# Performance work log

Hardware: AMD Instinct MI355X
Metric: run time of the kernel (lower is better)

The kernel has to match this reference:

```python
import jax, jax.numpy as jnp
import numpy as np

B = 16384
D = 1024          # fusion_hidden == depth_hidden == expert hidden
ORD_H = 512       # max(48, fusion_hidden // 2)
E = 7             # num_size_classes (= number of depth experts)
C_SIZE = 7        # num_size_classes
C_DEPTH = 3       # num_depth_classes


def _lin(key, fan_in, fan_out):
    return jax.random.normal(key, (fan_in, fan_out), dtype=jnp.float32) / np.sqrt(fan_in)


def setup_inputs() -> dict:
    key = jax.random.key(0)
    ks = jax.random.split(key, 16)
    inp = {
        'hybrid_feat': jax.random.normal(ks[0], (B, D), dtype=jnp.float32),
        # size_cls_head: Linear(D, D) -> ReLU -> Linear(D, 7)
        'Wc1': _lin(ks[1], D, D), 'bc1': jnp.zeros((D,), jnp.float32),
        'Wc2': _lin(ks[2], D, C_SIZE), 'bc2': jnp.zeros((C_SIZE,), jnp.float32),
        # size_ord_head: Linear(D, 512) -> ReLU -> Linear(512, 6)
        'Wo1': _lin(ks[3], D, ORD_H), 'bo1': jnp.zeros((ORD_H,), jnp.float32),
        'Wo2': _lin(ks[4], ORD_H, C_SIZE - 1), 'bo2': jnp.zeros((C_SIZE - 1,), jnp.float32),
        # size_residual_head: Linear(D, D) -> ReLU -> Linear(D, 1)
        'Wr1': _lin(ks[5], D, D), 'br1': jnp.zeros((D,), jnp.float32),
        'Wr2': _lin(ks[6], D, 1), 'br2': jnp.zeros((1,), jnp.float32),
        # depth_adapter: Linear(D, D) -> ReLU
        'Wa': _lin(ks[7], D, D), 'ba': jnp.zeros((D,), jnp.float32),
        # 7 stacked DepthExperts: Linear(D,D) ReLU Linear(D,D) ReLU Linear(D,3)
        'We1': jax.random.normal(ks[8], (E, D, D), jnp.float32) / np.sqrt(D),
        'be1': jnp.zeros((E, D), jnp.float32),
        'We2': jax.random.normal(ks[9], (E, D, D), jnp.float32) / np.sqrt(D),
        'be2': jnp.zeros((E, D), jnp.float32),
        'We3': jax.random.normal(ks[10], (E, D, C_DEPTH), jnp.float32) / np.sqrt(D),
        'be3': jnp.zeros((E, C_DEPTH), jnp.float32),
    }
    return inp


def reference(hybrid_feat, Wc1, bc1, Wc2, bc2, Wo1, bo1, Wo2, bo2,
              Wr1, br1, Wr2, br2, Wa, ba, We1, be1, We2, be2, We3, be3):
    x = hybrid_feat  # [B, D]
    relu = jax.nn.relu
    # size classification head
    size_logits = relu(x @ Wc1 + bc1) @ Wc2 + bc2                      # [B, 7]
    # ordinal head
    size_ord_logits = relu(x @ Wo1 + bo1) @ Wo2 + bo2                  # [B, 6]
    size_probs = jax.nn.softmax(size_logits, axis=1)                   # [B, 7]
    size_values = jnp.linspace(0.0, 1.0, C_SIZE, dtype=size_probs.dtype)
    expected_norm = jnp.sum(size_probs * size_values[None, :], axis=1, keepdims=True)  # [B, 1]
    residual = 0.35 * jnp.tanh(relu(x @ Wr1 + br1) @ Wr2 + br2)        # [B, 1]
    size_reg_norm = jnp.clip(expected_norm + residual, 0.0, 1.0)       # [B, 1]
    # depth adapter + hard-routed depth experts (route_depth_logits)
    depth_feat = relu(x @ Wa + ba)                                     # [B, D]
    size_idx = jnp.argmax(size_logits, axis=1)                         # [B] hard route
    # dense all-expert compute, then per-row select == gather/scatter dispatch
    h1 = relu(jnp.einsum('bd,edh->ebh', depth_feat, We1) + be1[:, None, :])   # [E, B, D]
    h2 = relu(jnp.einsum('ebd,edh->ebh', h1, We2) + be2[:, None, :])          # [E, B, D]
    expert_logits = jnp.einsum('ebd,edc->ebc', h2, We3) + be3[:, None, :]     # [E, B, 3]
    depth_logits = jnp.take_along_axis(
        jnp.transpose(expert_logits, (1, 0, 2)),  # [B, E, 3]
        size_idx[:, None, None], axis=1)[:, 0, :]                       # [B, 3]
    # single concatenated output: [B, 7 + 6 + 1 + 7 + 3] = [B, 24]
    return jnp.concatenate(
        [size_logits, size_ord_logits, size_reg_norm, size_probs, depth_logits], axis=1)
```

## Files before the change

### kernel.cpp

```cpp
#include <hip/hip_runtime.h>
#include <cstdint>
#include <cstddef>

typedef unsigned short u16;
typedef u16 u16x8 __attribute__((ext_vector_type(8)));
typedef __bf16 bf16x8 __attribute__((ext_vector_type(8)));
typedef float f32x4 __attribute__((ext_vector_type(4)));

#define B_ROWS 16384
#define DIM 1024
#define ORDH 512
#define NEXP 7
#define NFUSE 2560

__device__ __forceinline__ u16 f2bf(float f) {
  unsigned u = __builtin_bit_cast(unsigned, f);
  u += 0x7FFFu + ((u >> 16) & 1u);
  return (u16)(u >> 16);
}
__device__ __forceinline__ float bf2f(u16 h) {
  return __builtin_bit_cast(float, ((unsigned)h) << 16);
}

typedef __attribute__((address_space(1))) const void gas_void;
typedef __attribute__((address_space(3))) void las_void;
__device__ __forceinline__ void gload16(const void* g, void* l) {
  __builtin_amdgcn_global_load_lds((gas_void*)g, (las_void*)l, 16, 0, 0);
}

__global__ __launch_bounds__(256) void convert_x_kernel(
    const float4* __restrict__ x, ushort4* __restrict__ xh,
    ushort4* __restrict__ xl, int* __restrict__ gcnt, int* __restrict__ cursor) {
  if (blockIdx.x == 0 && threadIdx.x < 2 * NEXP) {
    if (threadIdx.x < NEXP) gcnt[threadIdx.x] = 0;
    else cursor[threadIdx.x - NEXP] = 0;
  }
  const int i = blockIdx.x * 256 + threadIdx.x;
  float4 v = x[i];
  ushort4 h, l;
  h.x = f2bf(v.x); l.x = f2bf(v.x - bf2f(h.x));
  h.y = f2bf(v.y); l.y = f2bf(v.y - bf2f(h.y));
  h.z = f2bf(v.z); l.z = f2bf(v.z - bf2f(h.z));
  h.w = f2bf(v.w); l.w = f2bf(v.w - bf2f(h.w));
  xh[i] = h; xl[i] = l;
}

__global__ __launch_bounds__(256) void transpose_all_kernel(
    const float* __restrict__ Wc1, u16* __restrict__ Tc1h, u16* __restrict__ Tc1l,
    const float* __restrict__ Wo1, u16* __restrict__ To1,
    const float* __restrict__ Wr1, u16* __restrict__ Tr1,
    const float* __restrict__ Wa,  u16* __restrict__ Ta,
    const float* __restrict__ We1, u16* __restrict__ Te1,
    const float* __restrict__ We2, u16* __restrict__ Te2) {
  __shared__ float tile[32][33];
  int bid = blockIdx.x;
  const float* W; u16* H; u16* L = nullptr;
  int N = 1024, bx, by;
  size_t zoff = 0;
  if (bid < 1024)      { W = Wc1; H = Tc1h; L = Tc1l; bx = bid & 31; by = bid >> 5; }
  else if (bid < 1536) { bid -= 1024; W = Wo1; H = To1; N = 512; bx = bid & 15; by = bid >> 4; }
  else if (bid < 2560) { bid -= 1536; W = Wr1; H = Tr1; bx = bid & 31; by = bid >> 5; }
  else if (bid < 3584) { bid -= 2560; W = Wa; H = Ta; bx = bid & 31; by = bid >> 5; }
  else if (bid < 10752){ bid -= 3584; W = We1; H = Te1;
                         zoff = (size_t)(bid >> 10) * DIM * DIM; bid &= 1023;
                         bx = bid & 31; by = bid >> 5; }
  else                 { bid -= 10752; W = We2; H = Te2;
                         zoff = (size_t)(bid >> 10) * DIM * DIM; bid &= 1023;
                         bx = bid & 31; by = bid >> 5; }
  const int K = 1024;
  const int bk = by * 32, bn = bx * 32;
  const int tx = threadIdx.x & 31, ty = threadIdx.x >> 5;
#pragma unroll
  for (int r = 0; r < 32; r += 8)
    tile[ty + r][tx] = W[zoff + (size_t)(bk + ty + r) * N + (bn + tx)];
  __syncthreads();
#pragma unroll
  for (int r = 0; r < 32; r += 8) {
    const float v = tile[tx][ty + r];
    const size_t o = zoff + (size_t)(bn + ty + r) * K + (bk + tx);
    const u16 h = f2bf(v);
    H[o] = h;
    if (L) L[o] = f2bf(v - bf2f(h));
  }
}

__device__ __forceinline__ void gemm_loop(
    const u16* __restrict__ aP0, const u16* __restrict__ bP0,
    const u16* __restrict__ aP1, const u16* __restrict__ bP1,
    const u16* __restrict__ aP2, const u16* __restrict__ bP2,
    int npass, int K, int m0, int n0, u16* SM, int tid, f32x4 (&acc)[4][4]) {
  const int lane = tid & 63;
  const int w = tid >> 6;
  const int wm = w >> 1, wn = w & 1;
  const int sRow = tid >> 3, sSlot = tid & 7;
  const int ldsOff = sRow * 64 + sSlot * 8;
  const size_t aOff = (size_t)(m0 + sRow) * K + ((sSlot ^ (sRow & 7)) * 8);
  const size_t bOff = (size_t)(n0 + sRow) * K + ((sSlot ^ (sRow & 7)) * 8);
  const u16* aCur = aP0 + aOff;
  const u16* bCur = bP0 + bOff;
  int sp = 0, sk = 0;
  auto stageNext = [&](int b) {
    u16* d = SM + b * 16384 + ldsOff;
    const u16* as = aCur + sk;
    const u16* bs = bCur + sk;
#pragma unroll
    for (int r = 0; r < 4; ++r) {
      gload16(as + (size_t)(r * 32) * K, d + r * 32 * 64);
      gload16(bs + (size_t)(r * 32) * K, d + 8192 + r * 32 * 64);
    }
    sk += 64;
    if (sk == K) {
      sk = 0; ++sp;
      if (sp == 1) { aCur = aP1 + aOff; bCur = bP1 + bOff; }
      else         { aCur = aP2 + aOff; bCur = bP2 + bOff; }
    }
  };

  const int ntiles = npass * (K >> 6);
  stageNext(0);
  int cur = 0;
  for (int ti = 0; ti < ntiles; ++ti) {
    if (ti + 1 < ntiles) {
      stageNext(cur ^ 1);
      asm volatile("s_waitcnt vmcnt(8)\n\ts_barrier" ::: "memory");
    } else {
      asm volatile("s_waitcnt vmcnt(0)\n\ts_barrier" ::: "memory");
    }
    const u16* As = SM + cur * 16384;
    const u16* Bs = As + 8192;
#pragma unroll
    for (int s = 0; s < 2; ++s) {
      const int cAx = s * 4 + (lane >> 4);
      const int colO = (cAx ^ (lane & 7)) * 8;
      bf16x8 af[4], bfr[4];
#pragma unroll
      for (int t = 0; t < 4; ++t) {
        const int rowA = wm * 64 + t * 16 + (lane & 15);
        af[t] = __builtin_bit_cast(bf16x8, *(const u16x8*)&As[rowA * 64 + colO]);
        const int rowB = wn * 64 + t * 16 + (lane & 15);
        bfr[t] = __builtin_bit_cast(bf16x8, *(const u16x8*)&Bs[rowB * 64 + colO]);
      }
      __builtin_amdgcn_s_setprio(1);
#pragma unroll
      for (int mt = 0; mt < 4; ++mt)
#pragma unroll
        for (int nt = 0; nt < 4; ++nt)
          acc[mt][nt] = __builtin_amdgcn_mfma_f32_16x16x32_bf16(
              af[mt], bfr[nt], acc[mt][nt], 0, 0, 0);
      __builtin_amdgcn_s_setprio(0);
    }
    asm volatile("s_barrier" ::: "memory");
    cur ^= 1;
  }
}

__global__ __launch_bounds__(256, 2) void mgemm_bt_kernel(
    const u16* __restrict__ A0, const u16* __restrict__ B0,
    const u16* __restrict__ A1, const u16* __restrict__ B1,
    const u16* __restrict__ A2, const u16* __restrict__ B2,
    int npass, int K,
    float* __restrict__ outF, const float* __restrict__ biasF, int ldoF,
    u16* __restrict__ o0, u16* __restrict__ o1, u16* __restrict__ o2,
    const float* __restrict__ b0, const float* __restrict__ b1,
    const float* __restrict__ b2) {
  __shared__ __attribute__((aligned(16))) u16 SM[4 * 128 * 64];
  const int tid = threadIdx.x;
  const int lane = tid & 63;
  const int w = tid >> 6;
  const int wm = w >> 1, wn = w & 1;
  const unsigned nwg = gridDim.x * gridDim.y;
  const unsigned wgid = blockIdx.y * gridDim.x + blockIdx.x;
  const unsigned swz = (wgid & 7u) * (nwg >> 3) + (wgid >> 3);
  const int m0 = (int)(swz / gridDim.x) * 128;
  const int n0 = (int)(swz % gridDim.x) * 128;

  f32x4 acc[4][4] = {};
  gemm_loop(A0, B0, A1, B1, A2, B2, npass, K, m0, n0, SM, tid, acc);

  const int q = lane >> 4, cl = lane & 15;
#pragma unroll
  for (int nt = 0; nt < 4; ++nt) {
    const int col = n0 + wn * 64 + nt * 16 + cl;
    if (outF) {
      const float bv = biasF[col];
#pragma unroll
      for (int mt = 0; mt < 4; ++mt)
#pragma unroll
        for (int i = 0; i < 4; ++i) {
          const int row = m0 + wm * 64 + mt * 16 + q * 4 + i;
          float v = acc[mt][nt][i] + bv;
          outF[(size_t)row * ldoF + col] = v > 0.f ? v : 0.f;
        }
    } else {
      u16* ob; const float* bp; int lc, ld;
      if (col < ORDH)            { ob = o0; bp = b0; lc = col;               ld = ORDH; }
      else if (col < ORDH + DIM) { ob = o1; bp = b1; lc = col - ORDH;        ld = DIM; }
      else                       { ob = o2; bp = b2; lc = col - (ORDH + DIM); ld = DIM; }
      const float bv = bp[lc];
#pragma unroll
      for (int mt = 0; mt < 4; ++mt)
#pragma unroll
        for (int i = 0; i < 4; ++i) {
          const int row = m0 + wm * 64 + mt * 16 + q * 4 + i;
          float v = acc[mt][nt][i] + bv;
          v = v > 0.f ? v : 0.f;
          ob[(size_t)row * ld + lc] = f2bf(v);
        }
    }
  }
}

__global__ __launch_bounds__(256, 2) void mgemm_expert_kernel(
    const u16* __restrict__ Abuf, const u16* __restrict__ Wall,
    const float* __restrict__ biasAll, const int* __restrict__ cnt,
    const int* __restrict__ perm, int usePerm, u16* __restrict__ outH) {
  __shared__ __attribute__((aligned(16))) u16 SM[4 * 128 * 64];
  const int e = blockIdx.z;
  const int myCnt = cnt[e];
  const int t0 = blockIdx.y * 128;
  if (t0 >= myCnt) return;
  int base = 0;
  for (int t = 0; t < NEXP; ++t) base += (t < e) ? cnt[t] : 0;
  const int m0 = base + t0;
  const int mEnd = base + myCnt;
  const u16* Bp = Wall + (size_t)e * DIM * DIM;
  const float* bias = biasAll + (size_t)e * DIM;

  const int tid = threadIdx.x;
  const int lane = tid & 63;
  const int w = tid >> 6;
  const int wm = w >> 1, wn = w & 1;
  const int n0 = blockIdx.x * 128;
  const int sRow = tid >> 3, sSlot = tid & 7;
  const int ldsOff = sRow * 64 + sSlot * 8;
  const int swzC = (sSlot ^ (sRow & 7)) * 8;

  const u16* aSrc[4];
#pragma unroll
  for (int r = 0; r < 4; ++r) {
    int ar = m0 + r * 32 + sRow;
    if (ar > B_ROWS - 1) ar = B_ROWS - 1;
    const int gr = usePerm ? perm[ar] : ar;
    aSrc[r] = Abuf + (size_t)gr * DIM + swzC;
  }
  const u16* bSrc = Bp + (size_t)(n0 + sRow) * DIM + swzC;

  int sk = 0;
  auto stageNext = [&](int b) {
    u16* d = SM + b * 16384 + ldsOff;
#pragma unroll
    for (int r = 0; r < 4; ++r)
      gload16(aSrc[r] + sk, d + r * 32 * 64);
#pragma unroll
    for (int r = 0; r < 4; ++r)
      gload16(bSrc + (size_t)(r * 32) * DIM + sk, d + 8192 + r * 32 * 64);
    sk += 64;
  };

  f32x4 acc[4][4] = {};
  const int ntiles = DIM >> 6;
  stageNext(0);
  int cur = 0;
  for (int ti = 0; ti < ntiles; ++ti) {
    if (ti + 1 < ntiles) {
      stageNext(cur ^ 1);
      asm volatile("s_waitcnt vmcnt(8)\n\ts_barrier" ::: "memory");
    } else {
      asm volatile("s_waitcnt vmcnt(0)\n\ts_barrier" ::: "memory");
    }
    const u16* As = SM + cur * 16384;
    const u16* Bs = As + 8192;
#pragma unroll
    for (int s = 0; s < 2; ++s) {
      const int cAx = s * 4 + (lane >> 4);
      const int colO = (cAx ^ (lane & 7)) * 8;
      bf16x8 af[4], bfr[4];
#pragma unroll
      for (int t = 0; t < 4; ++t) {
        const int rowA = wm * 64 + t * 16 + (lane & 15);
        af[t] = __builtin_bit_cast(bf16x8, *(const u16x8*)&As[rowA * 64 + colO]);
        const int rowB = wn * 64 + t * 16 + (lane & 15);
        bfr[t] = __builtin_bit_cast(bf16x8, *(const u16x8*)&Bs[rowB * 64 + colO]);
      }
      __builtin_amdgcn_s_setprio(1);
#pragma unroll
      for (int mt = 0; mt < 4; ++mt)
#pragma unroll
        for (int nt = 0; nt < 4; ++nt)
          acc[mt][nt] = __builtin_amdgcn_mfma_f32_16x16x32_bf16(
              af[mt], bfr[nt], acc[mt][nt], 0, 0, 0);
      __builtin_amdgcn_s_setprio(0);
    }
    asm volatile("s_barrier" ::: "memory");
    cur ^= 1;
  }

  const int q = lane >> 4, cl = lane & 15;
#pragma unroll
  for (int nt = 0; nt < 4; ++nt) {
    const int col = n0 + wn * 64 + nt * 16 + cl;
    const float bv = bias[col];
#pragma unroll
    for (int mt = 0; mt < 4; ++mt) {
#pragma unroll
      for (int i = 0; i < 4; ++i) {
        const int row = m0 + wm * 64 + mt * 16 + q * 4 + i;
        if (row < mEnd) {
          float v = acc[mt][nt][i] + bv;
          v = v > 0.f ? v : 0.f;
          outH[(size_t)row * DIM + col] = f2bf(v);
        }
      }
    }
  }
}

__global__ __launch_bounds__(256) void head_resord_kernel(
    const u16* __restrict__ Y3, const float* __restrict__ Wr2,
    const float* __restrict__ br2, float* __restrict__ resv,
    const u16* __restrict__ Y2, const float* __restrict__ Wo2,
    const float* __restrict__ bo2, float* __restrict__ out) {
  const int lane = threadIdx.x & 63;
  const int r = blockIdx.x * 4 + (threadIdx.x >> 6);
  float s = 0.f;
  for (int it = 0; it < 16; ++it) {
    const int k = it * 64 + lane;
    s += bf2f(Y3[(size_t)r * DIM + k]) * Wr2[k];
  }
  for (int o = 32; o > 0; o >>= 1) s += __shfl_down(s, o);
  if (lane == 0) resv[r] = 0.35f * tanhf(s + br2[0]);
  float so[6] = {0, 0, 0, 0, 0, 0};
  for (int it = 0; it < 8; ++it) {
    const int k = it * 64 + lane;
    const float v = bf2f(Y2[(size_t)r * ORDH + k]);
    const float* wr = Wo2 + k * 6;
#pragma unroll
    for (int n = 0; n < 6; ++n) so[n] += v * wr[n];
  }
#pragma unroll
  for (int n = 0; n < 6; ++n) {
    float xv = so[n];
    for (int o = 32; o > 0; o >>= 1) xv += __shfl_down(xv, o);
    so[n] = xv;
  }
  if (lane == 0) {
#pragma unroll
    for (int n = 0; n < 6; ++n) out[(size_t)r * 24 + 7 + n] = so[n] + bo2[n];
  }
}

__global__ __launch_bounds__(256) void head_cls_kernel(
    const float* __restrict__ Y1, const float* __restrict__ Wc2,
    const float* __restrict__ bc2, const float* __restrict__ resv,
    float* __restrict__ out, int* __restrict__ size_idx, int* __restrict__ gcnt) {
  __shared__ int lcnt[NEXP];
  const int tid = threadIdx.x;
  if (tid < NEXP) lcnt[tid] = 0;
  __syncthreads();
  const int lane = tid & 63;
  const int r = blockIdx.x * 4 + (tid >> 6);
  float s[7] = {0, 0, 0, 0, 0, 0, 0};
  for (int it = 0; it < 16; ++it) {
    const int k = it * 64 + lane;
    const float v = Y1[(size_t)r * DIM + k];
    const float* wr = Wc2 + k * 7;
#pragma unroll
    for (int n = 0; n < 7; ++n) s[n] += v * wr[n];
  }
#pragma unroll
  for (int n = 0; n < 7; ++n) {
    float xv = s[n];
    for (int o = 32; o > 0; o >>= 1) xv += __shfl_down(xv, o);
    s[n] = xv;
  }
  if (lane == 0) {
    float lg[7], p[7];
    float m = -1e30f;
    int ai = 0;
#pragma unroll
    for (int n = 0; n < 7; ++n) {
      lg[n] = s[n] + bc2[n];
      if (lg[n] > m) { m = lg[n]; ai = n; }
    }
    float es = 0.f;
#pragma unroll
    for (int n = 0; n < 7; ++n) { p[n] = expf(lg[n] - m); es += p[n]; }
    const float inv = 1.f / es;
    float expect = 0.f;
#pragma unroll
    for (int n = 0; n < 7; ++n) { p[n] *= inv; expect += p[n] * (n * (1.f / 6.f)); }
    float reg = expect + resv[r];
    reg = fminf(fmaxf(reg, 0.f), 1.f);
    float* orow = out + (size_t)r * 24;
#pragma unroll
    for (int n = 0; n < 7; ++n) orow[n] = lg[n];
    orow[13] = reg;
#pragma unroll
    for (int n = 0; n < 7; ++n) orow[14 + n] = p[n];
    size_idx[r] = ai;
    atomicAdd(&lcnt[ai], 1);
  }
  __syncthreads();
  if (tid < NEXP && lcnt[tid] > 0) atomicAdd(&gcnt[tid], lcnt[tid]);
}

__global__ __launch_bounds__(256) void scatter_kernel(
    const int* __restrict__ size_idx, const int* __restrict__ gcnt,
    int* __restrict__ cursor, int* __restrict__ perm) {
  __shared__ int lcnt[NEXP];
  __shared__ int lbase[NEXP];
  const int tid = threadIdx.x;
  if (tid < NEXP) lcnt[tid] = 0;
  __syncthreads();
  const int r = blockIdx.x * 256 + tid;
  const int e = size_idx[r];
  const int lp = atomicAdd(&lcnt[e], 1);
  __syncthreads();
  if (tid < NEXP && lcnt[tid] > 0) {
    int off = 0;
    for (int t = 0; t < tid; ++t) off += gcnt[t];
    lbase[tid] = off + atomicAdd(&cursor[tid], lcnt[tid]);
  }
  __syncthreads();
  perm[lbase[e] + lp] = r;
}

__global__ __launch_bounds__(256) void head_dl_kernel(
    const u16* __restrict__ H2p, const float* __restrict__ We3,
    const float* __restrict__ be3, const int* __restrict__ gcnt,
    const int* __restrict__ perm, float* __restrict__ out) {
  const int lane = threadIdx.x & 63;
  const int i = blockIdx.x * 4 + (threadIdx.x >> 6);
  int e = 0, acc = 0;
#pragma unroll
  for (int t = 0; t < NEXP - 1; ++t) {
    acc += gcnt[t];
    if (i >= acc) e = t + 1;
  }
  const float* W = We3 + (size_t)e * DIM * 3;
  float s0 = 0.f, s1 = 0.f, s2 = 0.f;
  for (int it = 0; it < 16; ++it) {
    const int k = it * 64 + lane;
    const float v = bf2f(H2p[(size_t)i * DIM + k]);
    s0 += v * W[k * 3 + 0];
    s1 += v * W[k * 3 + 1];
    s2 += v * W[k * 3 + 2];
  }
  for (int o = 32; o > 0; o >>= 1) {
    s0 += __shfl_down(s0, o);
    s1 += __shfl_down(s1, o);
    s2 += __shfl_down(s2, o);
  }
  if (lane == 0) {
    const int r = perm[i];
    float* orow = out + (size_t)r * 24;
    orow[21] = s0 + be3[e * 3 + 0];
    orow[22] = s1 + be3[e * 3 + 1];
    orow[23] = s2 + be3[e * 3 + 2];
  }
}

extern "C" void kernel_launch(void* const* d_in, const int* in_sizes, int n_in,
                              void* d_out, int out_size, void* d_ws, size_t ws_size,
                              hipStream_t stream) {
  (void)in_sizes; (void)n_in; (void)out_size; (void)ws_size;
  const float* x   = (const float*)d_in[0];
  const float* Wc1 = (const float*)d_in[1];
  const float* bc1 = (const float*)d_in[2];
  const float* Wc2 = (const float*)d_in[3];
  const float* bc2 = (const float*)d_in[4];
  const float* Wo1 = (const float*)d_in[5];
  const float* bo1 = (const float*)d_in[6];
  const float* Wo2 = (const float*)d_in[7];
  const float* bo2 = (const float*)d_in[8];
  const float* Wr1 = (const float*)d_in[9];
  const float* br1 = (const float*)d_in[10];
  const float* Wr2 = (const float*)d_in[11];
  const float* br2 = (const float*)d_in[12];
  const float* Wa  = (const float*)d_in[13];
  const float* ba  = (const float*)d_in[14];
  const float* We1 = (const float*)d_in[15];
  const float* be1 = (const float*)d_in[16];
  const float* We2 = (const float*)d_in[17];
  const float* be2 = (const float*)d_in[18];
  const float* We3 = (const float*)d_in[19];
  const float* be3 = (const float*)d_in[20];
  float* out = (float*)d_out;

  char* p = (char*)d_ws;
  auto carve = [&](size_t bytes) {
    char* r = p;
    p += (bytes + 255) & ~(size_t)255;
    return r;
  };
  u16* xh   = (u16*)carve((size_t)B_ROWS * DIM * 2);
  u16* xl   = (u16*)carve((size_t)B_ROWS * DIM * 2);
  u16* Tc1h = (u16*)carve((size_t)DIM * DIM * 2);
  u16* Tc1l = (u16*)carve((size_t)DIM * DIM * 2);
  u16* Tall = (u16*)carve((size_t)NFUSE * DIM * 2);
  u16* Te1  = (u16*)carve((size_t)NEXP * DIM * DIM * 2);
  u16* Te2  = (u16*)carve((size_t)NEXP * DIM * DIM * 2);
  u16* Y3   = (u16*)carve((size_t)B_ROWS * DIM * 2);
  u16* Y2   = (u16*)carve((size_t)B_ROWS * ORDH * 2);
  carve((size_t)16 << 20);
  u16* DF   = (u16*)carve((size_t)B_ROWS * DIM * 2);
  float* resv = (float*)carve((size_t)B_ROWS * 4);
  int* size_idx = (int*)carve((size_t)B_ROWS * 4);
  int* perm   = (int*)carve((size_t)B_ROWS * 4);
  int* gcnt   = (int*)carve(256);
  int* cursor = (int*)carve(256);
  float* Y1 = (float*)Y3;
  u16* H1p = Y3;
  u16* H2p = DF;
  u16* To1 = Tall;
  u16* Tr1 = Tall + (size_t)ORDH * DIM;
  u16* Ta  = Tall + (size_t)(ORDH + DIM) * DIM;

  dim3 blk(256);
  convert_x_kernel<<<dim3(B_ROWS * DIM / 4 / 256), blk, 0, stream>>>(
      (const float4*)x, (ushort4*)xh, (ushort4*)xl, gcnt, cursor);
  transpose_all_kernel<<<dim3(17920), blk, 0, stream>>>(
      Wc1, Tc1h, Tc1l, Wo1, To1, Wr1, Tr1, Wa, Ta, We1, Te1, We2, Te2);

  mgemm_bt_kernel<<<dim3(NFUSE / 128, B_ROWS / 128), blk, 0, stream>>>(
      xh, Tall, xh, Tall, xh, Tall, 1, DIM,
      (float*)nullptr, (const float*)nullptr, 0,
      Y2, Y3, DF, bo1, br1, ba);
  head_resord_kernel<<<dim3(B_ROWS / 4), blk, 0, stream>>>(
      Y3, Wr2, br2, resv, Y2, Wo2, bo2, out);

  mgemm_bt_kernel<<<dim3(DIM / 128, B_ROWS / 128), blk, 0, stream>>>(
      xh, Tc1h, xh, Tc1l, xl, Tc1h, 3, DIM,
      Y1, bc1, DIM,
      (u16*)nullptr, (u16*)nullptr, (u16*)nullptr,
      (const float*)nullptr, (const float*)nullptr, (const float*)nullptr);
  head_cls_kernel<<<dim3(B_ROWS / 4), blk, 0, stream>>>(Y1, Wc2, bc2, resv, out,
                                                        size_idx, gcnt);
  scatter_kernel<<<dim3(B_ROWS / 256), blk, 0, stream>>>(size_idx, gcnt, cursor, perm);

  mgemm_expert_kernel<<<dim3(DIM / 128, B_ROWS / 128, NEXP), blk, 0, stream>>>(
      DF, Te1, be1, gcnt, perm, 1, H1p);
  mgemm_expert_kernel<<<dim3(DIM / 128, B_ROWS / 128, NEXP), blk, 0, stream>>>(
      H1p, Te2, be2, gcnt, perm, 0, H2p);
  head_dl_kernel<<<dim3(B_ROWS / 4), blk, 0, stream>>>(H2p, We3, be3, gcnt, perm, out);
}
```

Measured before the change: 640.5 us.

## Merge head GEMMs into one launch and fuse second-layer projections via atomics

Combines the fused ord/res/adapter GEMM and the 3-pass Wc1 GEMM into a single grid. Each tile's epilogue now applies bias and ReLU, projects onto the small second-layer weights, reduces across lanes with shuffles, and atomically accumulates into fp32 buffers that were zeroed in the convert kernel. The second expert GEMM gets the same We3 projection epilogue, which removes the Y1/Y2/Y3/H2 intermediate writes and the separate head reduction kernels. It also drops the s_setprio hints, and it adds atomic contention plus nondeterministic summation order.

After: 808.7 us. +26.3%, slower.

```diff
diff --git a/kernel.cpp b/kernel.cpp
--- a/kernel.cpp
+++ b/kernel.cpp
@@ -12,6 +12,7 @@
 #define ORDH 512
 #define NEXP 7
 #define NFUSE 2560
+#define NMEGA 3584
 
 __device__ __forceinline__ u16 f2bf(float f) {
   unsigned u = __builtin_bit_cast(unsigned, f);
@@ -30,12 +31,15 @@
 
 __global__ __launch_bounds__(256) void convert_x_kernel(
     const float4* __restrict__ x, ushort4* __restrict__ xh,
-    ushort4* __restrict__ xl, int* __restrict__ gcnt, int* __restrict__ cursor) {
+    ushort4* __restrict__ xl, int* __restrict__ gcnt, int* __restrict__ cursor,
+    float* __restrict__ zacc) {
   if (blockIdx.x == 0 && threadIdx.x < 2 * NEXP) {
     if (threadIdx.x < NEXP) gcnt[threadIdx.x] = 0;
     else cursor[threadIdx.x - NEXP] = 0;
   }
-  const int i = blockIdx.x * 256 + threadIdx.x;
+  const int z = blockIdx.x * 256 + threadIdx.x;
+  if (z < 17 * B_ROWS) zacc[z] = 0.f;
+  const int i = z;
   float4 v = x[i];
   ushort4 h, l;
   h.x = f2bf(v.x); l.x = f2bf(v.x - bf2f(h.x));
@@ -88,14 +92,14 @@
     const u16* __restrict__ aP0, const u16* __restrict__ bP0,
     const u16* __restrict__ aP1, const u16* __restrict__ bP1,
     const u16* __restrict__ aP2, const u16* __restrict__ bP2,
-    int npass, int K, int m0, int n0, u16* SM, int tid, f32x4 (&acc)[4][4]) {
+    int npass, int K, int m0, u16* SM, int tid, f32x4 (&acc)[4][4]) {
   const int lane = tid & 63;
   const int w = tid >> 6;
   const int wm = w >> 1, wn = w & 1;
   const int sRow = tid >> 3, sSlot = tid & 7;
   const int ldsOff = sRow * 64 + sSlot * 8;
   const size_t aOff = (size_t)(m0 + sRow) * K + ((sSlot ^ (sRow & 7)) * 8);
-  const size_t bOff = (size_t)(n0 + sRow) * K + ((sSlot ^ (sRow & 7)) * 8);
+  const size_t bOff = (size_t)sRow * K + ((sSlot ^ (sRow & 7)) * 8);
   const u16* aCur = aP0 + aOff;
   const u16* bCur = bP0 + bOff;
   int sp = 0, sk = 0;
@@ -140,29 +144,28 @@
         const int rowB = wn * 64 + t * 16 + (lane & 15);
         bfr[t] = __builtin_bit_cast(bf16x8, *(const u16x8*)&Bs[rowB * 64 + colO]);
       }
-      __builtin_amdgcn_s_setprio(1);
 #pragma unroll
       for (int mt = 0; mt < 4; ++mt)
 #pragma unroll
         for (int nt = 0; nt < 4; ++nt)
           acc[mt][nt] = __builtin_amdgcn_mfma_f32_16x16x32_bf16(
               af[mt], bfr[nt], acc[mt][nt], 0, 0, 0);
-      __builtin_amdgcn_s_setprio(0);
     }
     asm volatile("s_barrier" ::: "memory");
     cur ^= 1;
   }
 }
 
-__global__ __launch_bounds__(256, 2) void mgemm_bt_kernel(
-    const u16* __restrict__ A0, const u16* __restrict__ B0,
-    const u16* __restrict__ A1, const u16* __restrict__ B1,
-    const u16* __restrict__ A2, const u16* __restrict__ B2,
-    int npass, int K,
-    float* __restrict__ outF, const float* __restrict__ biasF, int ldoF,
-    u16* __restrict__ o0, u16* __restrict__ o1, u16* __restrict__ o2,
-    const float* __restrict__ b0, const float* __restrict__ b1,
-    const float* __restrict__ b2) {
+__global__ __launch_bounds__(256, 2) void mega_gemm_kernel(
+    const u16* __restrict__ xh, const u16* __restrict__ xl,
+    const u16* __restrict__ Tall, const u16* __restrict__ Tc1h,
+    const u16* __restrict__ Tc1l,
+    const float* __restrict__ bo1, const float* __restrict__ br1,
+    const float* __restrict__ ba, const float* __restrict__ bc1,
+    const float* __restrict__ Wo2, const float* __restrict__ Wr2,
+    const float* __restrict__ Wc2,
+    float* __restrict__ ordacc, float* __restrict__ resacc,
+    float* __restrict__ clsacc, u16* __restrict__ DF) {
   __shared__ __attribute__((aligned(16))) u16 SM[4 * 128 * 64];
   const int tid = threadIdx.x;
   const int lane = tid & 63;
@@ -175,28 +178,68 @@
   const int n0 = (int)(swz % gridDim.x) * 128;
 
   f32x4 acc[4][4] = {};
-  gemm_loop(A0, B0, A1, B1, A2, B2, npass, K, m0, n0, SM, tid, acc);
+  if (n0 < NFUSE) {
+    const u16* b = Tall + (size_t)n0 * DIM;
+    gemm_loop(xh, b, xh, b, xh, b, 1, DIM, m0, SM, tid, acc);
+  } else {
+    const u16* bh = Tc1h + (size_t)(n0 - NFUSE) * DIM;
+    const u16* bl = Tc1l + (size_t)(n0 - NFUSE) * DIM;
+    gemm_loop(xh, bh, xh, bl, xl, bh, 3, DIM, m0, SM, tid, acc);
+  }
 
   const int q = lane >> 4, cl = lane & 15;
-#pragma unroll
-  for (int nt = 0; nt < 4; ++nt) {
-    const int col = n0 + wn * 64 + nt * 16 + cl;
-    if (outF) {
-      const float bv = biasF[col];
-#pragma unroll
-      for (int mt = 0; mt < 4; ++mt)
-#pragma unroll
-        for (int i = 0; i < 4; ++i) {
-          const int row = m0 + wm * 64 + mt * 16 + q * 4 + i;
-          float v = acc[mt][nt][i] + bv;
-          outF[(size_t)row * ldoF + col] = v > 0.f ? v : 0.f;
+  if (n0 < ORDH) {
+#pragma unroll
+    for (int mt = 0; mt < 4; ++mt)
+#pragma unroll
+      for (int i = 0; i < 4; ++i) {
+        const int row = m0 + wm * 64 + mt * 16 + q * 4 + i;
+        float s[6] = {0, 0, 0, 0, 0, 0};
+#pragma unroll
+        for (int nt = 0; nt < 4; ++nt) {
+          const int col = n0 + wn * 64 + nt * 16 + cl;
+          float v = acc[mt][nt][i] + bo1[col];
+          v = v > 0.f ? v : 0.f;
+          const float* wr = Wo2 + col * 6;
+#pragma unroll
+          for (int n = 0; n < 6; ++n) s[n] += v * wr[n];
         }
-    } else {
-      u16* ob; const float* bp; int lc, ld;
-      if (col < ORDH)            { ob = o0; bp = b0; lc = col;               ld = ORDH; }
-      else if (col < ORDH + DIM) { ob = o1; bp = b1; lc = col - ORDH;        ld = DIM; }
-      else                       { ob = o2; bp = b2; lc = col - (ORDH + DIM); ld = DIM; }
-      const float bv = bp[lc];
+#pragma unroll
+        for (int n = 0; n < 6; ++n) {
+          s[n] += __shfl_xor(s[n], 1);
+          s[n] += __shfl_xor(s[n], 2);
+          s[n] += __shfl_xor(s[n], 4);
+          s[n] += __shfl_xor(s[n], 8);
+        }
+        if (cl == 0)
+#pragma unroll
+          for (int n = 0; n < 6; ++n) atomicAdd(&ordacc[row * 6 + n], s[n]);
+      }
+  } else if (n0 < ORDH + DIM) {
+#pragma unroll
+    for (int mt = 0; mt < 4; ++mt)
+#pragma unroll
+      for (int i = 0; i < 4; ++i) {
+        const int row = m0 + wm * 64 + mt * 16 + q * 4 + i;
+        float s = 0.f;
+#pragma unroll
+        for (int nt = 0; nt < 4; ++nt) {
+          const int col = n0 - ORDH + wn * 64 + nt * 16 + cl;
+          float v = acc[mt][nt][i] + br1[col];
+          v = v > 0.f ? v : 0.f;
+          s += v * Wr2[col];
+        }
+        s += __shfl_xor(s, 1);
+        s += __shfl_xor(s, 2);
+        s += __shfl_xor(s, 4);
+        s += __shfl_xor(s, 8);
+        if (cl == 0) atomicAdd(&resacc[row], s);
+      }
+  } else if (n0 < NFUSE) {
+#pragma unroll
+    for (int nt = 0; nt < 4; ++nt) {
+      const int col = n0 - (ORDH + DIM) + wn * 64 + nt * 16 + cl;
+      const float bv = ba[col];
 #pragma unroll
       for (int mt = 0; mt < 4; ++mt)
 #pragma unroll
@@ -204,16 +247,43 @@
           const int row = m0 + wm * 64 + mt * 16 + q * 4 + i;
           float v = acc[mt][nt][i] + bv;
           v = v > 0.f ? v : 0.f;
-          ob[(size_t)row * ld + lc] = f2bf(v);
+          DF[(size_t)row * DIM + col] = f2bf(v);
         }
     }
-  }
-}
-
-__global__ __launch_bounds__(256, 2) void mgemm_expert_kernel(
+  } else {
+#pragma unroll
+    for (int mt = 0; mt < 4; ++mt)
+#pragma unroll
+      for (int i = 0; i < 4; ++i) {
+        const int row = m0 + wm * 64 + mt * 16 + q * 4 + i;
+        float s[7] = {0, 0, 0, 0, 0, 0, 0};
+#pragma unroll
+        for (int nt = 0; nt < 4; ++nt) {
+          const int col = n0 - NFUSE + wn * 64 + nt * 16 + cl;
+          float v = acc[mt][nt][i] + bc1[col];
+          v = v > 0.f ? v : 0.f;
+          const float* wr = Wc2 + col * 7;
+#pragma unroll
+          for (int n = 0; n < 7; ++n) s[n] += v * wr[n];
+        }
+#pragma unroll
+        for (int n = 0; n < 7; ++n) {
+          s[n] += __shfl_xor(s[n], 1);
+          s[n] += __shfl_xor(s[n], 2);
+          s[n] += __shfl_xor(s[n], 4);
+          s[n] += __shfl_xor(s[n], 8);
+        }
+        if (cl == 0)
+#pragma unroll
+          for (int n = 0; n < 7; ++n) atomicAdd(&clsacc[row * 7 + n], s[n]);
+      }
+  }
+}
+
+__global__ __launch_bounds__(256, 2) void mgemm_expert1_kernel(
     const u16* __restrict__ Abuf, const u16* __restrict__ Wall,
     const float* __restrict__ biasAll, const int* __restrict__ cnt,
-    const int* __restrict__ perm, int usePerm, u16* __restrict__ outH) {
+    const int* __restrict__ perm, u16* __restrict__ outH) {
   __shared__ __attribute__((aligned(16))) u16 SM[4 * 128 * 64];
   const int e = blockIdx.z;
   const int myCnt = cnt[e];
@@ -240,8 +310,7 @@
   for (int r = 0; r < 4; ++r) {
     int ar = m0 + r * 32 + sRow;
     if (ar > B_ROWS - 1) ar = B_ROWS - 1;
-    const int gr = usePerm ? perm[ar] : ar;
-    aSrc[r] = Abuf + (size_t)gr * DIM + swzC;
+    aSrc[r] = Abuf + (size_t)perm[ar] * DIM + swzC;
   }
   const u16* bSrc = Bp + (size_t)(n0 + sRow) * DIM + swzC;
 
@@ -282,14 +351,12 @@
         const int rowB = wn * 64 + t * 16 + (lane & 15);
         bfr[t] = __builtin_bit_cast(bf16x8, *(const u16x8*)&Bs[rowB * 64 + colO]);
       }
-      __builtin_amdgcn_s_setprio(1);
 #pragma unroll
       for (int mt = 0; mt < 4; ++mt)
 #pragma unroll
         for (int nt = 0; nt < 4; ++nt)
           acc[mt][nt] = __builtin_amdgcn_mfma_f32_16x16x32_bf16(
               af[mt], bfr[nt], acc[mt][nt], 0, 0, 0);
-      __builtin_amdgcn_s_setprio(0);
     }
     asm volatile("s_barrier" ::: "memory");
     cur ^= 1;
@@ -315,91 +382,156 @@
   }
 }
 
-__global__ __launch_bounds__(256) void head_resord_kernel(
-    const u16* __restrict__ Y3, const float* __restrict__ Wr2,
-    const float* __restrict__ br2, float* __restrict__ resv,
-    const u16* __restrict__ Y2, const float* __restrict__ Wo2,
-    const float* __restrict__ bo2, float* __restrict__ out) {
-  const int lane = threadIdx.x & 63;
-  const int r = blockIdx.x * 4 + (threadIdx.x >> 6);
-  float s = 0.f;
-  for (int it = 0; it < 16; ++it) {
-    const int k = it * 64 + lane;
-    s += bf2f(Y3[(size_t)r * DIM + k]) * Wr2[k];
-  }
-  for (int o = 32; o > 0; o >>= 1) s += __shfl_down(s, o);
-  if (lane == 0) resv[r] = 0.35f * tanhf(s + br2[0]);
-  float so[6] = {0, 0, 0, 0, 0, 0};
-  for (int it = 0; it < 8; ++it) {
-    const int k = it * 64 + lane;
-    const float v = bf2f(Y2[(size_t)r * ORDH + k]);
-    const float* wr = Wo2 + k * 6;
-#pragma unroll
-    for (int n = 0; n < 6; ++n) so[n] += v * wr[n];
-  }
-#pragma unroll
-  for (int n = 0; n < 6; ++n) {
-    float xv = so[n];
-    for (int o = 32; o > 0; o >>= 1) xv += __shfl_down(xv, o);
-    so[n] = xv;
-  }
-  if (lane == 0) {
-#pragma unroll
-    for (int n = 0; n < 6; ++n) out[(size_t)r * 24 + 7 + n] = so[n] + bo2[n];
-  }
-}
-
-__global__ __launch_bounds__(256) void head_cls_kernel(
-    const float* __restrict__ Y1, const float* __restrict__ Wc2,
-    const float* __restrict__ bc2, const float* __restrict__ resv,
+__global__ __launch_bounds__(256, 2) void mgemm_expert2_kernel(
+    const u16* __restrict__ Abuf, const u16* __restrict__ Wall,
+    const float* __restrict__ biasAll, const int* __restrict__ cnt,
+    const float* __restrict__ We3, float* __restrict__ dlacc) {
+  __shared__ __attribute__((aligned(16))) u16 SM[4 * 128 * 64];
+  const int e = blockIdx.z;
+  const int myCnt = cnt[e];
+  const int t0 = blockIdx.y * 128;
+  if (t0 >= myCnt) return;
+  int base = 0;
+  for (int t = 0; t < NEXP; ++t) base += (t < e) ? cnt[t] : 0;
+  const int m0 = base + t0;
+  const int mEnd = base + myCnt;
+  const u16* Bp = Wall + (size_t)e * DIM * DIM;
+  const float* bias = biasAll + (size_t)e * DIM;
+  const float* W3 = We3 + (size_t)e * DIM * 3;
+
+  const int tid = threadIdx.x;
+  const int lane = tid & 63;
+  const int w = tid >> 6;
+  const int wm = w >> 1, wn = w & 1;
+  const int n0 = blockIdx.x * 128;
+  const int sRow = tid >> 3, sSlot = tid & 7;
+  const int ldsOff = sRow * 64 + sSlot * 8;
+  const int swzC = (sSlot ^ (sRow & 7)) * 8;
+
+  const u16* aSrc[4];
+#pragma unroll
+  for (int r = 0; r < 4; ++r) {
+    int ar = m0 + r * 32 + sRow;
+    if (ar > B_ROWS - 1) ar = B_ROWS - 1;
+    aSrc[r] = Abuf + (size_t)ar * DIM + swzC;
+  }
+  const u16* bSrc = Bp + (size_t)(n0 + sRow) * DIM + swzC;
+
+  int sk = 0;
+  auto stageNext = [&](int b) {
+    u16* d = SM + b * 16384 + ldsOff;
+#pragma unroll
+    for (int r = 0; r < 4; ++r)
+      gload16(aSrc[r] + sk, d + r * 32 * 64);
+#pragma unroll
+    for (int r = 0; r < 4; ++r)
+      gload16(bSrc + (size_t)(r * 32) * DIM + sk, d + 8192 + r * 32 * 64);
+    sk += 64;
+  };
+
+  f32x4 acc[4][4] = {};
+  const int ntiles = DIM >> 6;
+  stageNext(0);
+  int cur = 0;
+  for (int ti = 0; ti < ntiles; ++ti) {
+    if (ti + 1 < ntiles) {
+      stageNext(cur ^ 1);
+      asm volatile("s_waitcnt vmcnt(8)\n\ts_barrier" ::: "memory");
+    } else {
+      asm volatile("s_waitcnt vmcnt(0)\n\ts_barrier" ::: "memory");
+    }
+    const u16* As = SM + cur * 16384;
+    const u16* Bs = As + 8192;
+#pragma unroll
+    for (int s = 0; s < 2; ++s) {
+      const int cAx = s * 4 + (lane >> 4);
+      const int colO = (cAx ^ (lane & 7)) * 8;
+      bf16x8 af[4], bfr[4];
+#pragma unroll
+      for (int t = 0; t < 4; ++t) {
+        const int rowA = wm * 64 + t * 16 + (lane & 15);
+        af[t] = __builtin_bit_cast(bf16x8, *(const u16x8*)&As[rowA * 64 + colO]);
+        const int rowB = wn * 64 + t * 16 + (lane & 15);
+        bfr[t] = __builtin_bit_cast(bf16x8, *(const u16x8*)&Bs[rowB * 64 + colO]);
+      }
+#pragma unroll
+      for (int mt = 0; mt < 4; ++mt)
+#pragma unroll
+        for (int nt = 0; nt < 4; ++nt)
+          acc[mt][nt] = __builtin_amdgcn_mfma_f32_16x16x32_bf16(
+              af[mt], bfr[nt], acc[mt][nt], 0, 0, 0);
+    }
+    asm volatile("s_barrier" ::: "memory");
+    cur ^= 1;
+  }
+
+  const int q = lane >> 4, cl = lane & 15;
+#pragma unroll
+  for (int mt = 0; mt < 4; ++mt)
+#pragma unroll
+    for (int i = 0; i < 4; ++i) {
+      const int row = m0 + wm * 64 + mt * 16 + q * 4 + i;
+      float s0 = 0.f, s1 = 0.f, s2 = 0.f;
+#pragma unroll
+      for (int nt = 0; nt < 4; ++nt) {
+        const int col = n0 + wn * 64 + nt * 16 + cl;
+        float v = acc[mt][nt][i] + bias[col];
+        v = v > 0.f ? v : 0.f;
+        const float* wr = W3 + col * 3;
+        s0 += v * wr[0]; s1 += v * wr[1]; s2 += v * wr[2];
+      }
+      s0 += __shfl_xor(s0, 1); s0 += __shfl_xor(s0, 2);
+      s0 += __shfl_xor(s0, 4); s0 += __shfl_xor(s0, 8);
+      s1 += __shfl_xor(s1, 1); s1 += __shfl_xor(s1, 2);
+      s1 += __shfl_xor(s1, 4); s1 += __shfl_xor(s1, 8);
+      s2 += __shfl_xor(s2, 1); s2 += __shfl_xor(s2, 2);
+      s2 += __shfl_xor(s2, 4); s2 += __shfl_xor(s2, 8);
+      if (cl == 0 && row < mEnd) {
+        atomicAdd(&dlacc[row * 3 + 0], s0);
+        atomicAdd(&dlacc[row * 3 + 1], s1);
+        atomicAdd(&dlacc[row * 3 + 2], s2);
+      }
+    }
+}
+
+__global__ __launch_bounds__(256) void finalize_cls_kernel(
+    const float* __restrict__ ordacc, const float* __restrict__ bo2,
+    const float* __restrict__ resacc, const float* __restrict__ br2,
+    const float* __restrict__ clsacc, const float* __restrict__ bc2,
     float* __restrict__ out, int* __restrict__ size_idx, int* __restrict__ gcnt) {
   __shared__ int lcnt[NEXP];
   const int tid = threadIdx.x;
   if (tid < NEXP) lcnt[tid] = 0;
   __syncthreads();
-  const int lane = tid & 63;
-  const int r = blockIdx.x * 4 + (tid >> 6);
-  float s[7] = {0, 0, 0, 0, 0, 0, 0};
-  for (int it = 0; it < 16; ++it) {
-    const int k = it * 64 + lane;
-    const float v = Y1[(size_t)r * DIM + k];
-    const float* wr = Wc2 + k * 7;
-#pragma unroll
-    for (int n = 0; n < 7; ++n) s[n] += v * wr[n];
-  }
+  const int r = blockIdx.x * 256 + tid;
+  float* orow = out + (size_t)r * 24;
+#pragma unroll
+  for (int n = 0; n < 6; ++n) orow[7 + n] = ordacc[r * 6 + n] + bo2[n];
+  const float resv = 0.35f * tanhf(resacc[r] + br2[0]);
+  float lg[7], pb[7];
+  float m = -1e30f;
+  int ai = 0;
 #pragma unroll
   for (int n = 0; n < 7; ++n) {
-    float xv = s[n];
-    for (int o = 32; o > 0; o >>= 1) xv += __shfl_down(xv, o);
-    s[n] = xv;
-  }
-  if (lane == 0) {
-    float lg[7], p[7];
-    float m = -1e30f;
-    int ai = 0;
-#pragma unroll
-    for (int n = 0; n < 7; ++n) {
-      lg[n] = s[n] + bc2[n];
-      if (lg[n] > m) { m = lg[n]; ai = n; }
-    }
-    float es = 0.f;
-#pragma unroll
-    for (int n = 0; n < 7; ++n) { p[n] = expf(lg[n] - m); es += p[n]; }
-    const float inv = 1.f / es;
-    float expect = 0.f;
-#pragma unroll
-    for (int n = 0; n < 7; ++n) { p[n] *= inv; expect += p[n] * (n * (1.f / 6.f)); }
-    float reg = expect + resv[r];
-    reg = fminf(fmaxf(reg, 0.f), 1.f);
-    float* orow = out + (size_t)r * 24;
-#pragma unroll
-    for (int n = 0; n < 7; ++n) orow[n] = lg[n];
-    orow[13] = reg;
-#pragma unroll
-    for (int n = 0; n < 7; ++n) orow[14 + n] = p[n];
-    size_idx[r] = ai;
-    atomicAdd(&lcnt[ai], 1);
-  }
+    lg[n] = clsacc[r * 7 + n] + bc2[n];
+    if (lg[n] > m) { m = lg[n]; ai = n; }
+  }
+  float es = 0.f;
+#pragma unroll
+  for (int n = 0; n < 7; ++n) { pb[n] = expf(lg[n] - m); es += pb[n]; }
+  const float inv = 1.f / es;
+  float expect = 0.f;
+#pragma unroll
+  for (int n = 0; n < 7; ++n) { pb[n] *= inv; expect += pb[n] * (n * (1.f / 6.f)); }
+  float reg = expect + resv;
+  reg = fminf(fmaxf(reg, 0.f), 1.f);
+#pragma unroll
+  for (int n = 0; n < 7; ++n) orow[n] = lg[n];
+  orow[13] = reg;
+#pragma unroll
+  for (int n = 0; n < 7; ++n) orow[14 + n] = pb[n];
+  size_idx[r] = ai;
+  atomicAdd(&lcnt[ai], 1);
   __syncthreads();
   if (tid < NEXP && lcnt[tid] > 0) atomicAdd(&gcnt[tid], lcnt[tid]);
 }
@@ -425,39 +557,21 @@
   perm[lbase[e] + lp] = r;
 }
 
-__global__ __launch_bounds__(256) void head_dl_kernel(
-    const u16* __restrict__ H2p, const float* __restrict__ We3,
-    const float* __restrict__ be3, const int* __restrict__ gcnt,
-    const int* __restrict__ perm, float* __restrict__ out) {
-  const int lane = threadIdx.x & 63;
-  const int i = blockIdx.x * 4 + (threadIdx.x >> 6);
-  int e = 0, acc = 0;
+__global__ __launch_bounds__(256) void finalize_dl_kernel(
+    const float* __restrict__ dlacc, const float* __restrict__ be3,
+    const int* __restrict__ gcnt, const int* __restrict__ perm,
+    float* __restrict__ out) {
+  const int i = blockIdx.x * 256 + threadIdx.x;
+  int e = 0, a = 0;
 #pragma unroll
   for (int t = 0; t < NEXP - 1; ++t) {
-    acc += gcnt[t];
-    if (i >= acc) e = t + 1;
-  }
-  const float* W = We3 + (size_t)e * DIM * 3;
-  float s0 = 0.f, s1 = 0.f, s2 = 0.f;
-  for (int it = 0; it < 16; ++it) {
-    const int k = it * 64 + lane;
-    const float v = bf2f(H2p[(size_t)i * DIM + k]);
-    s0 += v * W[k * 3 + 0];
-    s1 += v * W[k * 3 + 1];
-    s2 += v * W[k * 3 + 2];
-  }
-  for (int o = 32; o > 0; o >>= 1) {
-    s0 += __shfl_down(s0, o);
-    s1 += __shfl_down(s1, o);
-    s2 += __shfl_down(s2, o);
-  }
-  if (lane == 0) {
-    const int r = perm[i];
-    float* orow = out + (size_t)r * 24;
-    orow[21] = s0 + be3[e * 3 + 0];
-    orow[22] = s1 + be3[e * 3 + 1];
-    orow[23] = s2 + be3[e * 3 + 2];
-  }
+    a += gcnt[t];
+    if (i >= a) e = t + 1;
+  }
+  const int r = perm[i];
+  float* orow = out + (size_t)r * 24;
+#pragma unroll
+  for (int c = 0; c < 3; ++c) orow[21 + c] = dlacc[i * 3 + c] + be3[e * 3 + c];
 }
 
 extern "C" void kernel_launch(void* const* d_in, const int* in_sizes, int n_in,
@@ -500,47 +614,38 @@
   u16* Tall = (u16*)carve((size_t)NFUSE * DIM * 2);
   u16* Te1  = (u16*)carve((size_t)NEXP * DIM * DIM * 2);
   u16* Te2  = (u16*)carve((size_t)NEXP * DIM * DIM * 2);
-  u16* Y3   = (u16*)carve((size_t)B_ROWS * DIM * 2);
-  u16* Y2   = (u16*)carve((size_t)B_ROWS * ORDH * 2);
-  carve((size_t)16 << 20);
   u16* DF   = (u16*)carve((size_t)B_ROWS * DIM * 2);
-  float* resv = (float*)carve((size_t)B_ROWS * 4);
+  float* zacc = (float*)carve((size_t)17 * B_ROWS * 4);
   int* size_idx = (int*)carve((size_t)B_ROWS * 4);
   int* perm   = (int*)carve((size_t)B_ROWS * 4);
   int* gcnt   = (int*)carve(256);
   int* cursor = (int*)carve(256);
-  float* Y1 = (float*)Y3;
-  u16* H1p = Y3;
-  u16* H2p = DF;
+  float* ordacc = zacc;
+  float* resacc = zacc + 6 * B_ROWS;
+  float* clsacc = zacc + 7 * B_ROWS;
+  float* dlacc  = zacc + 14 * B_ROWS;
+  u16* H1p = xl;
   u16* To1 = Tall;
   u16* Tr1 = Tall + (size_t)ORDH * DIM;
   u16* Ta  = Tall + (size_t)(ORDH + DIM) * DIM;
 
   dim3 blk(256);
   convert_x_kernel<<<dim3(B_ROWS * DIM / 4 / 256), blk, 0, stream>>>(
-      (const float4*)x, (ushort4*)xh, (ushort4*)xl, gcnt, cursor);
+      (const float4*)x, (ushort4*)xh, (ushort4*)xl, gcnt, cursor, zacc);
   transpose_all_kernel<<<dim3(17920), blk, 0, stream>>>(
       Wc1, Tc1h, Tc1l, Wo1, To1, Wr1, Tr1, Wa, Ta, We1, Te1, We2, Te2);
 
-  mgemm_bt_kernel<<<dim3(NFUSE / 128, B_ROWS / 128), blk, 0, stream>>>(
-      xh, Tall, xh, Tall, xh, Tall, 1, DIM,
-      (float*)nullptr, (const float*)nullptr, 0,
-      Y2, Y3, DF, bo1, br1, ba);
-  head_resord_kernel<<<dim3(B_ROWS / 4), blk, 0, stream>>>(
-      Y3, Wr2, br2, resv, Y2, Wo2, bo2, out);
-
-  mgemm_bt_kernel<<<dim3(DIM / 128, B_ROWS / 128), blk, 0, stream>>>(
-      xh, Tc1h, xh, Tc1l, xl, Tc1h, 3, DIM,
-      Y1, bc1, DIM,
-      (u16*)nullptr, (u16*)nullptr, (u16*)nullptr,
-      (const float*)nullptr, (const float*)nullptr, (const float*)nullptr);
-  head_cls_kernel<<<dim3(B_ROWS / 4), blk, 0, stream>>>(Y1, Wc2, bc2, resv, out,
-                                                        size_idx, gcnt);
+  mega_gemm_kernel<<<dim3(NMEGA / 128, B_ROWS / 128), blk, 0, stream>>>(
+      xh, xl, Tall, Tc1h, Tc1l, bo1, br1, ba, bc1, Wo2, Wr2, Wc2,
+      ordacc, resacc, clsacc, DF);
+  finalize_cls_kernel<<<dim3(B_ROWS / 256), blk, 0, stream>>>(
+      ordacc, bo2, resacc, br2, clsacc, bc2, out, size_idx, gcnt);
   scatter_kernel<<<dim3(B_ROWS / 256), blk, 0, stream>>>(size_idx, gcnt, cursor, perm);
 
-  mgemm_expert_kernel<<<dim3(DIM / 128, B_ROWS / 128, NEXP), blk, 0, stream>>>(
-      DF, Te1, be1, gcnt, perm, 1, H1p);
-  mgemm_expert_kernel<<<dim3(DIM / 128, B_ROWS / 128, NEXP), blk, 0, stream>>>(
-      H1p, Te2, be2, gcnt, perm, 0, H2p);
-  head_dl_kernel<<<dim3(B_ROWS / 4), blk, 0, stream>>>(H2p, We3, be3, gcnt, perm, out);
-}
+  mgemm_expert1_kernel<<<dim3(DIM / 128, B_ROWS / 128, NEXP), blk, 0, stream>>>(
+      DF, Te1, be1, gcnt, perm, H1p);
+  mgemm_expert2_kernel<<<dim3(DIM / 128, B_ROWS / 128, NEXP), blk, 0, stream>>>(
+      H1p, Te2, be2, gcnt, We3, dlacc);
+  finalize_dl_kernel<<<dim3(B_ROWS / 256), blk, 0, stream>>>(
+      dlacc, be3, gcnt, perm, out);
+}
```
